# Optimization experiments

Hardware: AMD Instinct MI355X
Metric: run time of the kernel (lower is better)

Reference implementation:

```python
import jax, jax.numpy as jnp
import numpy as np

KSTRIDE = (16, 16)  # matches init_kwargs kstride


def setup_inputs() -> dict:
    key = jax.random.key(0)
    k1, k2, k3, k4, k5 = jax.random.split(key, 5)
    B, C, H, W = 4, 64, 512, 512
    N, kh, kw = 2048, 16, 16
    sh, sw = KSTRIDE
    inp = jax.random.normal(k1, (B, C, H, W), dtype=jnp.float32)
    gathered = jax.random.normal(k2, (N, C, kh, kw), dtype=jnp.float32)
    # valid block coords: h0*sh + kh <= H  ->  h0 in [0, H//sh) since kh == sh
    bi = jax.random.randint(k3, (N,), 0, B)
    hi = jax.random.randint(k4, (N,), 0, H // sh)
    wi = jax.random.randint(k5, (N,), 0, W // sw)
    indices = jnp.stack([bi, hi, wi], axis=1).astype(jnp.int64)
    return {"input": inp, "gathered": gathered, "indices": indices}


def reference(input, gathered, indices):
    # Vectorized scatter-add of N patches [C, kh, kw] into input [B, C, H, W]
    # at strided block offsets. Duplicated indices accumulate (+=), matching
    # the original in-place loop.
    sh, sw = KSTRIDE
    N, C, kh, kw = gathered.shape
    b = indices[:, 0][:, None, None]                                   # [N,1,1]
    r = (indices[:, 1] * sh)[:, None, None] + jnp.arange(kh)[None, :, None]  # [N,kh,1]
    c = (indices[:, 2] * sw)[:, None, None] + jnp.arange(kw)[None, None, :]  # [N,1,kw]
    x = jnp.transpose(input, (0, 2, 3, 1))      # [B,H,W,C] so C is a trailing slice
    g = jnp.transpose(gathered, (0, 2, 3, 1))   # [N,kh,kw,C]
    x = x.at[b, r, c, :].add(g)                 # scatter-add over all N blocks at once
    return jnp.transpose(x, (0, 3, 1, 2))       # back to [B,C,H,W]
```

## Files before the change

kernel.cpp:

```cpp
#include <hip/hip_runtime.h>

#define BB 4
#define CC 64
#define HH 512
#define WW 512
#define NN 2048
#define SLOTS 4096


__global__ void init_ws_kernel(int* __restrict__ heads, int* __restrict__ flag) {
    int i = blockIdx.x * blockDim.x + threadIdx.x;
    if (i < SLOTS) heads[i] = -1;
    if (i == 0) *flag = 1;
}

__global__ void detect_dtype_kernel(const int* __restrict__ idx32,
                                    int* __restrict__ flag) {
    int i = blockIdx.x * blockDim.x + threadIdx.x;
    if (i < 3 * NN / 2) {
        if (idx32[2 * i + 1] != 0) *flag = 0;
    }
}

__global__ void build_lists_kernel(const int* __restrict__ idx,
                                   int* __restrict__ heads,
                                   int* __restrict__ nxt,
                                   const int* __restrict__ flag) {
    int n = blockIdx.x * blockDim.x + threadIdx.x;
    if (n < NN) {
        int b, hi, wi;
        if (*flag) {
            b  = idx[6 * n + 0];
            hi = idx[6 * n + 2];
            wi = idx[6 * n + 4];
        } else {
            b  = idx[3 * n + 0];
            hi = idx[3 * n + 1];
            wi = idx[3 * n + 2];
        }
        int slot = (b << 10) | (hi << 5) | wi;
        nxt[n] = atomicExch(&heads[slot], n);
    }
}

__global__ __launch_bounds__(256) void scatter_add_kernel(
    const float4* __restrict__ in4,
    const float4* __restrict__ g4,
    const int* __restrict__ heads,
    const int* __restrict__ nxt,
    float4* __restrict__ out4)
{
    int e = blockIdx.x * 256 + threadIdx.x;
    const int w4 = e & 127;
    const int h  = (e >> 7) & 511;
    const int cb = e >> 16;
    const int c  = cb & 63;
    const int b  = cb >> 6;

    float4 v = in4[e];

    const int slot = (b << 10) | ((h >> 4) << 5) | (w4 >> 2);
    int n = heads[slot];
    if (n >= 0) {
        const int goff4 = (c << 6) | ((h & 15) << 2) | (w4 & 3);
        do {
            float4 g = g4[n * 4096 + goff4];
            v.x += g.x; v.y += g.y; v.z += g.z; v.w += g.w;
            n = nxt[n];
        } while (n >= 0);
    }
    out4[e] = v;
}

__global__ __launch_bounds__(256) void copy_kernel(const float4* __restrict__ in4,
                                                   float4* __restrict__ out4) {
    int e = blockIdx.x * 256 + threadIdx.x;
    out4[e] = in4[e];
}

__global__ __launch_bounds__(256) void atomic_scatter_kernel(
    const float* __restrict__ g,
    const int* __restrict__ idx,
    float* __restrict__ out)
{
    int i = blockIdx.x * 256 + threadIdx.x;
    int n = i >> 14;
    int r = i & 16383;
    int c  = r >> 8;
    int rr = (r >> 4) & 15;
    int w  = r & 15;
    int b  = idx[3 * n + 0];
    int hi = idx[3 * n + 1];
    int wi = idx[3 * n + 2];
    int off = ((b * CC + c) * HH + hi * 16 + rr) * WW + wi * 16 + w;
    atomicAdd(&out[off], g[i]);
}

extern "C" void kernel_launch(void* const* d_in, const int* in_sizes, int n_in,
                              void* d_out, int out_size, void* d_ws, size_t ws_size,
                              hipStream_t stream) {
    const float* inp      = (const float*)d_in[0];
    const float* gathered = (const float*)d_in[1];
    const int*   idx      = (const int*)d_in[2];
    float* out = (float*)d_out;

    const size_t ws_needed = (size_t)(SLOTS + NN + 1) * sizeof(int);

    if (ws_size >= ws_needed) {
        int* heads = (int*)d_ws;
        int* nxt   = heads + SLOTS;
        int* flag  = nxt + NN;
        init_ws_kernel<<<(SLOTS + 255) / 256, 256, 0, stream>>>(heads, flag);
        detect_dtype_kernel<<<(3 * NN / 2 + 255) / 256, 256, 0, stream>>>(idx, flag);
        build_lists_kernel<<<(NN + 255) / 256, 256, 0, stream>>>(idx, heads, nxt, flag);
        const int n_out4 = BB * CC * HH * (WW / 4);
        scatter_add_kernel<<<n_out4 / 256, 256, 0, stream>>>(
            (const float4*)inp, (const float4*)gathered, heads, nxt, (float4*)out);
    } else {
        const int n_out4 = BB * CC * HH * (WW / 4);
        copy_kernel<<<n_out4 / 256, 256, 0, stream>>>((const float4*)inp, (float4*)out);
        const int n_g = NN * CC * 16 * 16;
        atomic_scatter_kernel<<<n_g / 256, 256, 0, stream>>>(gathered, idx, out);
    }
}
```

Before: 508.8 us.

## Fuse prelude kernels into one block and process four rows per thread

Merges the workspace init, index dtype detection and list-building kernels into one single-block kernel, using a shared flag and block syncs instead of three launches. The scatter-add kernel now handles four rows of float4 per thread, so one head lookup and one list walk are shared across four outputs and the gathered loads can be issued together. This cuts launch overhead and repeated linked-list traversal, at the cost of fewer threads and a serialized single-block prelude.

```diff
diff --git a/kernel.cpp b/kernel.cpp
--- a/kernel.cpp
+++ b/kernel.cpp
@@ -8,28 +8,26 @@
 #define SLOTS 4096
 
 
-__global__ void init_ws_kernel(int* __restrict__ heads, int* __restrict__ flag) {
-    int i = blockIdx.x * blockDim.x + threadIdx.x;
-    if (i < SLOTS) heads[i] = -1;
-    if (i == 0) *flag = 1;
-}
+__global__ __launch_bounds__(1024) void prelude_kernel(const int* __restrict__ idx,
+                                                       int* __restrict__ heads,
+                                                       int* __restrict__ nxt) {
+    __shared__ int s_is64;
+    const int t = threadIdx.x;
+    if (t == 0) s_is64 = 1;
 
-__global__ void detect_dtype_kernel(const int* __restrict__ idx32,
-                                    int* __restrict__ flag) {
-    int i = blockIdx.x * blockDim.x + threadIdx.x;
-    if (i < 3 * NN / 2) {
-        if (idx32[2 * i + 1] != 0) *flag = 0;
+    #pragma unroll
+    for (int i = t; i < SLOTS; i += 1024) heads[i] = -1;
+    __syncthreads();
+
+    for (int i = t; i < 3 * NN / 2; i += 1024) {
+        if (idx[2 * i + 1] != 0) s_is64 = 0;
     }
-}
+    __syncthreads();
 
-__global__ void build_lists_kernel(const int* __restrict__ idx,
-                                   int* __restrict__ heads,
-                                   int* __restrict__ nxt,
-                                   const int* __restrict__ flag) {
-    int n = blockIdx.x * blockDim.x + threadIdx.x;
-    if (n < NN) {
+    const bool is64 = (s_is64 != 0);
+    for (int n = t; n < NN; n += 1024) {
         int b, hi, wi;
-        if (*flag) {
+        if (is64) {
             b  = idx[6 * n + 0];
             hi = idx[6 * n + 2];
             wi = idx[6 * n + 4];
@@ -38,7 +36,7 @@
             hi = idx[3 * n + 1];
             wi = idx[3 * n + 2];
         }
-        int slot = (b << 10) | (hi << 5) | wi;
+        const int slot = (b << 10) | (hi << 5) | wi;
         nxt[n] = atomicExch(&heads[slot], n);
     }
 }
@@ -50,26 +48,44 @@
     const int* __restrict__ nxt,
     float4* __restrict__ out4)
 {
-    int e = blockIdx.x * 256 + threadIdx.x;
-    const int w4 = e & 127;
-    const int h  = (e >> 7) & 511;
-    const int cb = e >> 16;
+    const int t  = blockIdx.x * 256 + threadIdx.x;
+    const int w4 = t & 127;
+    const int hq = (t >> 7) & 127;
+    const int cb = t >> 14;
     const int c  = cb & 63;
     const int b  = cb >> 6;
+    const int h0 = hq << 2;
 
-    float4 v = in4[e];
+    const int base = (cb << 16) | (h0 << 7) | w4;
 
-    const int slot = (b << 10) | ((h >> 4) << 5) | (w4 >> 2);
+    float4 v0 = in4[base];
+    float4 v1 = in4[base + 128];
+    float4 v2 = in4[base + 256];
+    float4 v3 = in4[base + 384];
+
+    const int slot = (b << 10) | ((hq >> 2) << 5) | (w4 >> 2);
     int n = heads[slot];
     if (n >= 0) {
-        const int goff4 = (c << 6) | ((h & 15) << 2) | (w4 & 3);
+        const int goff = (c << 6) | ((h0 & 15) << 2) | (w4 & 3);
         do {
-            float4 g = g4[n * 4096 + goff4];
-            v.x += g.x; v.y += g.y; v.z += g.z; v.w += g.w;
-            n = nxt[n];
+            const float4* __restrict__ gp = g4 + ((n << 12) + goff);
+            const float4 g0 = gp[0];
+            const float4 g1 = gp[4];
+            const float4 g2 = gp[8];
+            const float4 g3 = gp[12];
+            const int nn = nxt[n];
+            v0.x += g0.x; v0.y += g0.y; v0.z += g0.z; v0.w += g0.w;
+            v1.x += g1.x; v1.y += g1.y; v1.z += g1.z; v1.w += g1.w;
+            v2.x += g2.x; v2.y += g2.y; v2.z += g2.z; v2.w += g2.w;
+            v3.x += g3.x; v3.y += g3.y; v3.z += g3.z; v3.w += g3.w;
+            n = nn;
         } while (n >= 0);
     }
-    out4[e] = v;
+
+    out4[base]       = v0;
+    out4[base + 128] = v1;
+    out4[base + 256] = v2;
+    out4[base + 384] = v3;
 }
 
 __global__ __launch_bounds__(256) void copy_kernel(const float4* __restrict__ in4,
@@ -104,17 +120,14 @@
     const int*   idx      = (const int*)d_in[2];
     float* out = (float*)d_out;
 
-    const size_t ws_needed = (size_t)(SLOTS + NN + 1) * sizeof(int);
+    const size_t ws_needed = (size_t)(SLOTS + NN) * sizeof(int);
 
     if (ws_size >= ws_needed) {
         int* heads = (int*)d_ws;
         int* nxt   = heads + SLOTS;
-        int* flag  = nxt + NN;
-        init_ws_kernel<<<(SLOTS + 255) / 256, 256, 0, stream>>>(heads, flag);
-        detect_dtype_kernel<<<(3 * NN / 2 + 255) / 256, 256, 0, stream>>>(idx, flag);
-        build_lists_kernel<<<(NN + 255) / 256, 256, 0, stream>>>(idx, heads, nxt, flag);
-        const int n_out4 = BB * CC * HH * (WW / 4);
-        scatter_add_kernel<<<n_out4 / 256, 256, 0, stream>>>(
+        prelude_kernel<<<1, 1024, 0, stream>>>(idx, heads, nxt);
+        const int n_thr = BB * CC * (HH / 4) * (WW / 4);
+        scatter_add_kernel<<<n_thr / 256, 256, 0, stream>>>(
             (const float4*)inp, (const float4*)gathered, heads, nxt, (float4*)out);
     } else {
         const int n_out4 = BB * CC * HH * (WW / 4);
```

After: 517.7 us. No clear change (+1.8%).
